# Kernel optimization log

Measured on AMD Instinct MI355X. Metric: run time of the kernel, lower is better.

The kernel has to match this reference:

```python
import jax, jax.numpy as jnp
import numpy as np

TAU = 0.1

def setup_inputs() -> dict:
    key = jax.random.key(0)
    kZ, k1, k2 = jax.random.split(key, 3)
    N, D = 8192, 128
    scale = 1.0 / np.sqrt(D)
    return {
        "Z": jax.random.normal(kZ, (N, D), dtype=jnp.float32),
        "W1": jax.random.normal(k1, (D, D), dtype=jnp.float32) * scale,
        "b1": jnp.zeros((D,), dtype=jnp.float32),
        "W2": jax.random.normal(k2, (D, D), dtype=jnp.float32) * scale,
        "b2": jnp.zeros((D,), dtype=jnp.float32),
    }

def reference(Z, W1, b1, W2, b2):
    # DiffusivityTransform: 2-layer MLP with ReLU (torch Linear: x @ W.T + b;
    # here W1/W2 are stored already transposed as [in, out])
    t = jax.nn.relu(Z @ W1 + b1) @ W2 + b2          # [N, D]
    sim = t @ t.T                                     # [N, N]
    S = jax.nn.softmax(sim, axis=1)                   # row-stochastic [N, N]
    Z_prop = S @ Z                                    # [N, D]
    return Z + TAU * (Z_prop - Z)
```

## Files before the change

### kernel.cpp

```cpp
#include <hip/hip_runtime.h>

typedef _Float16 half_t;
typedef _Float16 hx8 __attribute__((ext_vector_type(8)));
typedef _Float16 hx4 __attribute__((ext_vector_type(4)));
typedef float fx4 __attribute__((ext_vector_type(4)));

#define LOG2E 1.44269504088896f
#define TAU 0.1f
#define NSPLIT 8

__global__ __launch_bounds__(256) void mlpz_kernel(
    const float* __restrict__ Z, const float* __restrict__ W1,
    const float* __restrict__ b1, const float* __restrict__ W2,
    const float* __restrict__ b2, half_t* __restrict__ T,
    half_t* __restrict__ Zth)
{
  __shared__ float Ztile[16*132];
  __shared__ half_t Hs[16*136];
  const int tid = threadIdx.x;
  const int w = tid >> 6, lane = tid & 63;
  const int q = lane >> 4, c = lane & 15;
  const int rb = blockIdx.x*16;

#pragma unroll
  for (int i=0;i<2;++i) {
    int fid = i*256 + tid;
    int r = fid >> 5, c4 = (fid & 31)*4;
    *(fx4*)(&Ztile[r*132 + c4]) = *(const fx4*)(Z + (size_t)(rb + r)*128 + c4);
  }
  __syncthreads();

  {
    const int d = tid & 127, h = tid >> 7;
    hx8 hv;
#pragma unroll
    for (int u=0;u<8;++u) hv[u] = (half_t)Ztile[(h*8 + u)*132 + d];
    *(hx8*)(Zth + (size_t)d*8192 + rb + h*8) = hv;
  }

  hx8 zb[4];
#pragma unroll
  for (int ks=0;ks<4;++ks) {
    fx4 a = *(const fx4*)(&Ztile[c*132 + ks*32 + q*8]);
    fx4 b = *(const fx4*)(&Ztile[c*132 + ks*32 + q*8 + 4]);
#pragma unroll
    for (int u=0;u<4;++u) { zb[ks][u] = (half_t)a[u]; zb[ks][4+u] = (half_t)b[u]; }
  }

#pragma unroll
  for (int m2=0;m2<2;++m2) {
    const int mt = w*2 + m2;
    fx4 acc = (fx4){0.f,0.f,0.f,0.f};
#pragma unroll
    for (int ks=0;ks<4;++ks) {
      hx8 aw;
#pragma unroll
      for (int j=0;j<8;++j)
        aw[j] = (half_t)W1[(size_t)(ks*32 + q*8 + j)*128 + mt*16 + c];
      acc = __builtin_amdgcn_mfma_f32_16x16x32_f16(aw, zb[ks], acc, 0,0,0);
    }
    fx4 bias = *(const fx4*)(b1 + mt*16 + 4*q);
    hx4 hv;
#pragma unroll
    for (int i=0;i<4;++i) {
      float h = acc[i] + bias[i];
      hv[i] = (half_t)(h > 0.f ? h : 0.f);
    }
    *(hx4*)(&Hs[c*136 + mt*16 + 4*q]) = hv;
  }
  __syncthreads();

  hx8 hb[4];
#pragma unroll
  for (int ks=0;ks<4;++ks) hb[ks] = *(const hx8*)(&Hs[c*136 + ks*32 + q*8]);
#pragma unroll
  for (int m2=0;m2<2;++m2) {
    const int mt = w*2 + m2;
    fx4 acc = (fx4){0.f,0.f,0.f,0.f};
#pragma unroll
    for (int ks=0;ks<4;++ks) {
      hx8 aw;
#pragma unroll
      for (int j=0;j<8;++j)
        aw[j] = (half_t)W2[(size_t)(ks*32 + q*8 + j)*128 + mt*16 + c];
      acc = __builtin_amdgcn_mfma_f32_16x16x32_f16(aw, hb[ks], acc, 0,0,0);
    }
    fx4 bias = *(const fx4*)(b2 + mt*16 + 4*q);
    hx4 tv;
#pragma unroll
    for (int i=0;i<4;++i) tv[i] = (half_t)(acc[i] + bias[i]);
    *(hx4*)(T + (size_t)(rb + c)*128 + mt*16 + 4*q) = tv;
  }
}

__global__ __launch_bounds__(256,2) void flash_kernel(
    const half_t* __restrict__ T, const half_t* __restrict__ Zt,
    half_t* __restrict__ Pacc, float* __restrict__ Pm, float* __restrict__ Pl)
{
  __shared__ half_t Tbuf[2][8*512];
  __shared__ half_t Zbuf[2][8*512];
  const int tid = threadIdx.x;
  const int w = tid >> 6, lane = tid & 63;
  const int q = lane >> 4, c = lane & 15;
  const int bx = blockIdx.x;
  const int qb = bx >> 3, kh = bx & 7;
  const int wrow = qb*128 + w*32;
  const int sw = (c & 3) * 8;

  hx8 bq[2][4];
#pragma unroll
  for (int nt=0;nt<2;++nt)
#pragma unroll
    for (int ks=0;ks<4;++ks)
      bq[nt][ks] = *(const hx8*)(T + (size_t)(wrow + nt*16 + c)*128 + ks*32 + q*8);

  fx4 oacc[8][2];
#pragma unroll
  for (int mtd=0;mtd<8;++mtd)
#pragma unroll
    for (int nt=0;nt<2;++nt) oacc[mtd][nt] = (fx4){0.f,0.f,0.f,0.f};
  float m_run[2] = {-1e30f,-1e30f};
  float l_run[2] = {0.f,0.f};

  const int kbase = kh*1024;

  auto issue_loads = [&](int kt0, int b) {
    if (w < 2) {
#pragma unroll
      for (int i=0;i<4;++i) {
        int f = w*4 + i, mt = f >> 2, ks = f & 3;
        const half_t* gp = T + (size_t)(kt0 + mt*16 + c)*128 + ks*32 + q*8;
        half_t* lp = &Tbuf[b][f*512 + lane*8];
        __builtin_amdgcn_global_load_lds(
            (const __attribute__((address_space(1))) void*)gp,
            (__attribute__((address_space(3))) void*)lp, 16, 0, 0);
      }
    } else {
#pragma unroll
      for (int i=0;i<4;++i) {
        int f2 = (w-2)*4 + i;
        const half_t* gp = Zt + (size_t)(f2*16 + c)*8192 + kt0 + q*8;
        half_t* lp = &Zbuf[b][f2*512 + lane*8];
        __builtin_amdgcn_global_load_lds(
            (const __attribute__((address_space(1))) void*)gp,
            (__attribute__((address_space(3))) void*)lp, 16, 0, 0);
      }
    }
  };

  issue_loads(kbase, 0);

  for (int t=0;t<32;++t) {
    const int cur = t & 1;
    __syncthreads();
    half_t* Tcur = Tbuf[cur];
    half_t* Zcur = Zbuf[cur];
    half_t* Psw  = &Tbuf[cur][w*1024];

    fx4 sacc[2][2];
#pragma unroll
    for (int mt=0;mt<2;++mt)
#pragma unroll
      for (int nt=0;nt<2;++nt) sacc[mt][nt] = (fx4){0.f,0.f,0.f,0.f};
#pragma unroll
    for (int ks=0;ks<4;++ks)
#pragma unroll
      for (int mt=0;mt<2;++mt) {
        hx8 ak = *(const hx8*)(&Tcur[(mt*4+ks)*512 + lane*8]);
        sacc[mt][0] = __builtin_amdgcn_mfma_f32_16x16x32_f16(ak, bq[0][ks], sacc[mt][0], 0,0,0);
        sacc[mt][1] = __builtin_amdgcn_mfma_f32_16x16x32_f16(ak, bq[1][ks], sacc[mt][1], 0,0,0);
      }

    hx4 pk[2][2];
#pragma unroll
    for (int nt=0;nt<2;++nt) {
      float mx = -1e30f;
#pragma unroll
      for (int mt=0;mt<2;++mt)
#pragma unroll
        for (int i=0;i<4;++i) mx = fmaxf(mx, sacc[mt][nt][i]);
      mx = fmaxf(mx, __shfl_xor(mx, 16, 64));
      mx = fmaxf(mx, __shfl_xor(mx, 32, 64));
      float mnew = fmaxf(m_run[nt], mx);
      float alpha = __builtin_amdgcn_exp2f((m_run[nt]-mnew)*LOG2E);
      m_run[nt] = mnew;
      float nb = mnew*LOG2E;
      float rs = 0.f;
#pragma unroll
      for (int mt=0;mt<2;++mt) {
#pragma unroll
        for (int i=0;i<4;++i) {
          float p = __builtin_amdgcn_exp2f(sacc[mt][nt][i]*LOG2E - nb);
          rs += p;
          pk[nt][mt][i] = (half_t)p;
        }
      }
      rs += __shfl_xor(rs, 16, 64);
      rs += __shfl_xor(rs, 32, 64);
      l_run[nt] = l_run[nt]*alpha + rs;
#pragma unroll
      for (int mtd=0;mtd<8;++mtd)
#pragma unroll
        for (int i=0;i<4;++i) oacc[mtd][nt][i] *= alpha;
    }

    __syncthreads();
    if (t < 31) issue_loads(kbase + (t+1)*32, cur ^ 1);

#pragma unroll
    for (int nt=0;nt<2;++nt)
#pragma unroll
      for (int mt=0;mt<2;++mt)
        *(hx4*)(&Psw[(nt*16 + c)*32 + ((mt*16 + 4*q) ^ sw)]) = pk[nt][mt];

    {
      hx8 bp0 = *(const hx8*)(&Psw[(c     )*32 + ((q*8) ^ sw)]);
      hx8 bp1 = *(const hx8*)(&Psw[(16 + c)*32 + ((q*8) ^ sw)]);
#pragma unroll
      for (int mtd=0;mtd<8;++mtd) {
        hx8 az = *(const hx8*)(&Zcur[mtd*512 + lane*8]);
        oacc[mtd][0] = __builtin_amdgcn_mfma_f32_16x16x32_f16(az, bp0, oacc[mtd][0], 0,0,0);
        oacc[mtd][1] = __builtin_amdgcn_mfma_f32_16x16x32_f16(az, bp1, oacc[mtd][1], 0,0,0);
      }
    }
  }

#pragma unroll
  for (int nt=0;nt<2;++nt) {
    float inv = 1.0f / l_run[nt];
    const size_t rowg = (size_t)(bx*128 + w*32 + nt*16 + c);
#pragma unroll
    for (int mtd=0;mtd<8;++mtd) {
      hx4 ov;
#pragma unroll
      for (int i=0;i<4;++i) ov[i] = (half_t)(oacc[mtd][nt][i]*inv);
      *(hx4*)(Pacc + rowg*128 + mtd*16 + 4*q) = ov;
    }
    if (q == 0) {
      Pm[rowg] = m_run[nt];
      Pl[rowg] = l_run[nt];
    }
  }
}

__global__ __launch_bounds__(256) void merge_kernel(
    const float* __restrict__ Z, const half_t* __restrict__ Pacc,
    const float* __restrict__ Pm, const float* __restrict__ Pl,
    float* __restrict__ out)
{
  const int th = blockIdx.x*256 + threadIdx.x;
  const int r = th >> 5, cg = th & 31;
  const int qb = r >> 7, rr = r & 127;
  float mk[NSPLIT], lk[NSPLIT];
  float M = -1e30f;
#pragma unroll
  for (int k=0;k<NSPLIT;++k) {
    int p = qb*NSPLIT + k;
    mk[k] = Pm[p*128 + rr];
    lk[k] = Pl[p*128 + rr];
    M = fmaxf(M, mk[k]);
  }
  float L = 0.f, wk[NSPLIT];
#pragma unroll
  for (int k=0;k<NSPLIT;++k) { wk[k] = lk[k]*__builtin_amdgcn_exp2f((mk[k]-M)*LOG2E); L += wk[k]; }
  float o0=0.f,o1=0.f,o2=0.f,o3=0.f;
#pragma unroll
  for (int k=0;k<NSPLIT;++k) {
    int p = qb*NSPLIT + k;
    hx4 v = *(const hx4*)(Pacc + ((size_t)p*128 + rr)*128 + cg*4);
    o0 += wk[k]*(float)v[0]; o1 += wk[k]*(float)v[1];
    o2 += wk[k]*(float)v[2]; o3 += wk[k]*(float)v[3];
  }
  float invL = 1.0f / L;
  fx4 zv = *(const fx4*)(Z + (size_t)r*128 + cg*4);
  fx4 res;
  res[0] = (1.f-TAU)*zv[0] + TAU*o0*invL;
  res[1] = (1.f-TAU)*zv[1] + TAU*o1*invL;
  res[2] = (1.f-TAU)*zv[2] + TAU*o2*invL;
  res[3] = (1.f-TAU)*zv[3] + TAU*o3*invL;
  *(fx4*)(out + (size_t)r*128 + cg*4) = res;
}

extern "C" void kernel_launch(void* const* d_in, const int* in_sizes, int n_in,
                              void* d_out, int out_size, void* d_ws, size_t ws_size,
                              hipStream_t stream) {
  const float* Z  = (const float*)d_in[0];
  const float* W1 = (const float*)d_in[1];
  const float* b1 = (const float*)d_in[2];
  const float* W2 = (const float*)d_in[3];
  const float* b2 = (const float*)d_in[4];
  float* out = (float*)d_out;

  char* ws = (char*)d_ws;
  const size_t NBLK = 64 * NSPLIT;
  half_t* Thi  = (half_t*)(ws);
  half_t* Zth  = (half_t*)(ws + (size_t)2*1024*1024);
  half_t* Pacc = (half_t*)(ws + (size_t)4*1024*1024);
  float*  Pm   = (float*)(ws + (size_t)4*1024*1024 + NBLK*128*128*2);
  float*  Pl   = Pm + NBLK*128;

  hipLaunchKernelGGL(mlpz_kernel,  dim3(512),  dim3(256), 0, stream, Z, W1, b1, W2, b2, Thi, Zth);
  hipLaunchKernelGGL(flash_kernel, dim3(NBLK), dim3(256), 0, stream, Thi, Zth, Pacc, Pm, Pl);
  hipLaunchKernelGGL(merge_kernel, dim3(1024), dim3(256), 0, stream, Z, Pacc, Pm, Pl, out);
}
```

Baseline: 138.9 us.

## Prepack MLP weights to fp16, double flash key tile, add lazy softmax rescale

Adds a small kernel that packs W1/W2 into fp16 MFMA fragment order, so the MLP kernel loads each fragment with one vector load instead of eight strided scalar loads. The flash kernel now processes 64 keys per iteration instead of 32, which halves the barrier and loop count, doubles the LDS buffers and widens the P swizzle. It also skips the running-max update and accumulator rescale when the new tile max stays within 8 of the current max. That threshold bounds the growth of the unnormalized fp32 accumulators and fp16 P values, and it adds an extra launch and more LDS use per block.

```diff
diff --git a/kernel.cpp b/kernel.cpp
--- a/kernel.cpp
+++ b/kernel.cpp
@@ -9,9 +9,28 @@
 #define TAU 0.1f
 #define NSPLIT 8
 
+__global__ __launch_bounds__(256) void wpack_kernel(
+    const float* __restrict__ W1, const float* __restrict__ W2,
+    half_t* __restrict__ Wh1, half_t* __restrict__ Wh2)
+{
+  const int job = blockIdx.x*256 + threadIdx.x;
+  const int lane = job & 63;
+  const int frag = (job >> 6) & 31;
+  const int mat  = job >> 11;
+  const int mt = frag >> 2, ks = frag & 3;
+  const int q = lane >> 4, c = lane & 15;
+  const float* W = mat ? W2 : W1;
+  half_t* Wh = mat ? Wh2 : Wh1;
+  hx8 v;
+#pragma unroll
+  for (int j=0;j<8;++j)
+    v[j] = (half_t)W[(size_t)(ks*32 + q*8 + j)*128 + mt*16 + c];
+  *(hx8*)(Wh + ((size_t)frag*64 + lane)*8) = v;
+}
+
 __global__ __launch_bounds__(256) void mlpz_kernel(
-    const float* __restrict__ Z, const float* __restrict__ W1,
-    const float* __restrict__ b1, const float* __restrict__ W2,
+    const float* __restrict__ Z, const half_t* __restrict__ Wh1,
+    const float* __restrict__ b1, const half_t* __restrict__ Wh2,
     const float* __restrict__ b2, half_t* __restrict__ T,
     half_t* __restrict__ Zth)
 {
@@ -53,10 +72,7 @@
     fx4 acc = (fx4){0.f,0.f,0.f,0.f};
 #pragma unroll
     for (int ks=0;ks<4;++ks) {
-      hx8 aw;
-#pragma unroll
-      for (int j=0;j<8;++j)
-        aw[j] = (half_t)W1[(size_t)(ks*32 + q*8 + j)*128 + mt*16 + c];
+      hx8 aw = *(const hx8*)(Wh1 + ((size_t)(mt*4 + ks)*64 + lane)*8);
       acc = __builtin_amdgcn_mfma_f32_16x16x32_f16(aw, zb[ks], acc, 0,0,0);
     }
     fx4 bias = *(const fx4*)(b1 + mt*16 + 4*q);
@@ -79,10 +95,7 @@
     fx4 acc = (fx4){0.f,0.f,0.f,0.f};
 #pragma unroll
     for (int ks=0;ks<4;++ks) {
-      hx8 aw;
-#pragma unroll
-      for (int j=0;j<8;++j)
-        aw[j] = (half_t)W2[(size_t)(ks*32 + q*8 + j)*128 + mt*16 + c];
+      hx8 aw = *(const hx8*)(Wh2 + ((size_t)(mt*4 + ks)*64 + lane)*8);
       acc = __builtin_amdgcn_mfma_f32_16x16x32_f16(aw, hb[ks], acc, 0,0,0);
     }
     fx4 bias = *(const fx4*)(b2 + mt*16 + 4*q);
@@ -97,15 +110,15 @@
     const half_t* __restrict__ T, const half_t* __restrict__ Zt,
     half_t* __restrict__ Pacc, float* __restrict__ Pm, float* __restrict__ Pl)
 {
-  __shared__ half_t Tbuf[2][8*512];
-  __shared__ half_t Zbuf[2][8*512];
+  __shared__ half_t Tbuf[2][16*512];
+  __shared__ half_t Zbuf[2][16*512];
   const int tid = threadIdx.x;
   const int w = tid >> 6, lane = tid & 63;
   const int q = lane >> 4, c = lane & 15;
   const int bx = blockIdx.x;
   const int qb = bx >> 3, kh = bx & 7;
   const int wrow = qb*128 + w*32;
-  const int sw = (c & 3) * 8;
+  const int sw = (c & 7) * 8;
 
   hx8 bq[2][4];
 #pragma unroll
@@ -127,8 +140,8 @@
   auto issue_loads = [&](int kt0, int b) {
     if (w < 2) {
 #pragma unroll
-      for (int i=0;i<4;++i) {
-        int f = w*4 + i, mt = f >> 2, ks = f & 3;
+      for (int i=0;i<8;++i) {
+        int f = w*8 + i, mt = f >> 2, ks = f & 3;
         const half_t* gp = T + (size_t)(kt0 + mt*16 + c)*128 + ks*32 + q*8;
         half_t* lp = &Tbuf[b][f*512 + lane*8];
         __builtin_amdgcn_global_load_lds(
@@ -137,9 +150,9 @@
       }
     } else {
 #pragma unroll
-      for (int i=0;i<4;++i) {
-        int f2 = (w-2)*4 + i;
-        const half_t* gp = Zt + (size_t)(f2*16 + c)*8192 + kt0 + q*8;
+      for (int i=0;i<8;++i) {
+        int f2 = (w-2)*8 + i, mtd = f2 >> 1, ks2 = f2 & 1;
+        const half_t* gp = Zt + (size_t)(mtd*16 + c)*8192 + kt0 + ks2*32 + q*8;
         half_t* lp = &Zbuf[b][f2*512 + lane*8];
         __builtin_amdgcn_global_load_lds(
             (const __attribute__((address_space(1))) void*)gp,
@@ -150,75 +163,93 @@
 
   issue_loads(kbase, 0);
 
-  for (int t=0;t<32;++t) {
+  for (int t=0;t<16;++t) {
     const int cur = t & 1;
     __syncthreads();
     half_t* Tcur = Tbuf[cur];
     half_t* Zcur = Zbuf[cur];
-    half_t* Psw  = &Tbuf[cur][w*1024];
-
-    fx4 sacc[2][2];
-#pragma unroll
-    for (int mt=0;mt<2;++mt)
+    half_t* Psw  = &Tbuf[cur][w*2048];
+
+    fx4 sacc[4][2];
+#pragma unroll
+    for (int mt=0;mt<4;++mt)
 #pragma unroll
       for (int nt=0;nt<2;++nt) sacc[mt][nt] = (fx4){0.f,0.f,0.f,0.f};
 #pragma unroll
     for (int ks=0;ks<4;++ks)
 #pragma unroll
-      for (int mt=0;mt<2;++mt) {
+      for (int mt=0;mt<4;++mt) {
         hx8 ak = *(const hx8*)(&Tcur[(mt*4+ks)*512 + lane*8]);
         sacc[mt][0] = __builtin_amdgcn_mfma_f32_16x16x32_f16(ak, bq[0][ks], sacc[mt][0], 0,0,0);
         sacc[mt][1] = __builtin_amdgcn_mfma_f32_16x16x32_f16(ak, bq[1][ks], sacc[mt][1], 0,0,0);
       }
 
-    hx4 pk[2][2];
+    hx4 pk[2][4];
 #pragma unroll
     for (int nt=0;nt<2;++nt) {
       float mx = -1e30f;
 #pragma unroll
-      for (int mt=0;mt<2;++mt)
+      for (int mt=0;mt<4;++mt)
 #pragma unroll
         for (int i=0;i<4;++i) mx = fmaxf(mx, sacc[mt][nt][i]);
       mx = fmaxf(mx, __shfl_xor(mx, 16, 64));
       mx = fmaxf(mx, __shfl_xor(mx, 32, 64));
-      float mnew = fmaxf(m_run[nt], mx);
-      float alpha = __builtin_amdgcn_exp2f((m_run[nt]-mnew)*LOG2E);
-      m_run[nt] = mnew;
-      float nb = mnew*LOG2E;
-      float rs = 0.f;
-#pragma unroll
-      for (int mt=0;mt<2;++mt) {
-#pragma unroll
-        for (int i=0;i<4;++i) {
-          float p = __builtin_amdgcn_exp2f(sacc[mt][nt][i]*LOG2E - nb);
-          rs += p;
-          pk[nt][mt][i] = (half_t)p;
+      if (__all(mx <= m_run[nt] + 8.0f)) {
+        float nb = m_run[nt]*LOG2E;
+        float rs = 0.f;
+#pragma unroll
+        for (int mt=0;mt<4;++mt) {
+#pragma unroll
+          for (int i=0;i<4;++i) {
+            float p = __builtin_amdgcn_exp2f(sacc[mt][nt][i]*LOG2E - nb);
+            rs += p;
+            pk[nt][mt][i] = (half_t)p;
+          }
         }
-      }
-      rs += __shfl_xor(rs, 16, 64);
-      rs += __shfl_xor(rs, 32, 64);
-      l_run[nt] = l_run[nt]*alpha + rs;
-#pragma unroll
-      for (int mtd=0;mtd<8;++mtd)
-#pragma unroll
-        for (int i=0;i<4;++i) oacc[mtd][nt][i] *= alpha;
+        rs += __shfl_xor(rs, 16, 64);
+        rs += __shfl_xor(rs, 32, 64);
+        l_run[nt] += rs;
+      } else {
+        float mnew = fmaxf(m_run[nt], mx);
+        float alpha = __builtin_amdgcn_exp2f((m_run[nt]-mnew)*LOG2E);
+        m_run[nt] = mnew;
+        float nb = mnew*LOG2E;
+        float rs = 0.f;
+#pragma unroll
+        for (int mt=0;mt<4;++mt) {
+#pragma unroll
+          for (int i=0;i<4;++i) {
+            float p = __builtin_amdgcn_exp2f(sacc[mt][nt][i]*LOG2E - nb);
+            rs += p;
+            pk[nt][mt][i] = (half_t)p;
+          }
+        }
+        rs += __shfl_xor(rs, 16, 64);
+        rs += __shfl_xor(rs, 32, 64);
+        l_run[nt] = l_run[nt]*alpha + rs;
+#pragma unroll
+        for (int mtd=0;mtd<8;++mtd)
+#pragma unroll
+          for (int i=0;i<4;++i) oacc[mtd][nt][i] *= alpha;
+      }
     }
 
     __syncthreads();
-    if (t < 31) issue_loads(kbase + (t+1)*32, cur ^ 1);
+    if (t < 15) issue_loads(kbase + (t+1)*64, cur ^ 1);
 
 #pragma unroll
     for (int nt=0;nt<2;++nt)
 #pragma unroll
-      for (int mt=0;mt<2;++mt)
-        *(hx4*)(&Psw[(nt*16 + c)*32 + ((mt*16 + 4*q) ^ sw)]) = pk[nt][mt];
-
-    {
-      hx8 bp0 = *(const hx8*)(&Psw[(c     )*32 + ((q*8) ^ sw)]);
-      hx8 bp1 = *(const hx8*)(&Psw[(16 + c)*32 + ((q*8) ^ sw)]);
+      for (int mt=0;mt<4;++mt)
+        *(hx4*)(&Psw[(nt*16 + c)*64 + ((mt*16 + 4*q) ^ sw)]) = pk[nt][mt];
+
+#pragma unroll
+    for (int ks2=0;ks2<2;++ks2) {
+      hx8 bp0 = *(const hx8*)(&Psw[(c     )*64 + ((ks2*32 + q*8) ^ sw)]);
+      hx8 bp1 = *(const hx8*)(&Psw[(16 + c)*64 + ((ks2*32 + q*8) ^ sw)]);
 #pragma unroll
       for (int mtd=0;mtd<8;++mtd) {
-        hx8 az = *(const hx8*)(&Zcur[mtd*512 + lane*8]);
+        hx8 az = *(const hx8*)(&Zcur[(mtd*2+ks2)*512 + lane*8]);
         oacc[mtd][0] = __builtin_amdgcn_mfma_f32_16x16x32_f16(az, bp0, oacc[mtd][0], 0,0,0);
         oacc[mtd][1] = __builtin_amdgcn_mfma_f32_16x16x32_f16(az, bp1, oacc[mtd][1], 0,0,0);
       }
@@ -298,8 +329,11 @@
   half_t* Pacc = (half_t*)(ws + (size_t)4*1024*1024);
   float*  Pm   = (float*)(ws + (size_t)4*1024*1024 + NBLK*128*128*2);
   float*  Pl   = Pm + NBLK*128;
-
-  hipLaunchKernelGGL(mlpz_kernel,  dim3(512),  dim3(256), 0, stream, Z, W1, b1, W2, b2, Thi, Zth);
+  half_t* Wh1  = (half_t*)(ws + (size_t)20*1024*1024 + 512*1024);
+  half_t* Wh2  = Wh1 + 32*64*8;
+
+  hipLaunchKernelGGL(wpack_kernel, dim3(16),   dim3(256), 0, stream, W1, W2, Wh1, Wh2);
+  hipLaunchKernelGGL(mlpz_kernel,  dim3(512),  dim3(256), 0, stream, Z, Wh1, b1, Wh2, b2, Thi, Zth);
   hipLaunchKernelGGL(flash_kernel, dim3(NBLK), dim3(256), 0, stream, Thi, Zth, Pacc, Pm, Pl);
   hipLaunchKernelGGL(merge_kernel, dim3(1024), dim3(256), 0, stream, Z, Pacc, Pm, Pl, out);
 }
```

Measured after the change: 131.9 us. -5.0%, faster.
